# Kernel tuning notes

Measured on AMD Instinct MI355X. Metric: run time of the kernel, lower is better.

## Reference

```python
import jax, jax.numpy as jnp
import numpy as np

N, E, IN, HID, OUT, H, R = 50000, 800000, 128, 64, 64, 4, 64
NEG_SLOPE = 0.2


def setup_inputs() -> dict:
    key = jax.random.key(0)
    ks = jax.random.split(key, 20)
    s = 0.05
    inp = {
        "x": jax.random.normal(ks[0], (N, IN), jnp.float32),
        "edge_index": jax.random.randint(ks[1], (2, E), 0, N, jnp.int32),
        "edge_type": jax.random.randint(ks[2], (E,), 0, R, jnp.int32),
        # layer 1 (in -> hidden)
        "rel1": jax.random.normal(ks[3], (R, IN), jnp.float32) * s,
        "W1": jax.random.normal(ks[4], (IN, H * HID), jnp.float32) * s,
        "We1": jax.random.normal(ks[5], (IN, H * HID), jnp.float32) * s,
        "as1": jax.random.normal(ks[6], (H, HID), jnp.float32) * s,
        "ad1": jax.random.normal(ks[7], (H, HID), jnp.float32) * s,
        "ae1": jax.random.normal(ks[8], (H, HID), jnp.float32) * s,
        "b1": jnp.zeros((HID,), jnp.float32),
        # layer 2 (hidden -> out)
        "rel2": jax.random.normal(ks[9], (R, HID), jnp.float32) * s,
        "W2": jax.random.normal(ks[10], (HID, H * OUT), jnp.float32) * s,
        "We2": jax.random.normal(ks[11], (HID, H * OUT), jnp.float32) * s,
        "as2": jax.random.normal(ks[12], (H, OUT), jnp.float32) * s,
        "ad2": jax.random.normal(ks[13], (H, OUT), jnp.float32) * s,
        "ae2": jax.random.normal(ks[14], (H, OUT), jnp.float32) * s,
        "b2": jnp.zeros((OUT,), jnp.float32),
    }
    return inp


def gat_layer(x, src, dst, edge_type, rel, W, We, a_s, a_d, a_e, b, C):
    # x: [N, Din] -> per-head features [N, H, C]
    xs = (x @ W).reshape(-1, H, C)
    alpha_src = jnp.einsum('nhc,hc->nh', xs, a_s)   # [N,H]
    alpha_dst = jnp.einsum('nhc,hc->nh', xs, a_d)   # [N,H]
    e = (rel[edge_type] @ We).reshape(-1, H, C)     # [E,H,C] projected edge feats
    alpha_e = jnp.einsum('ehc,hc->eh', e, a_e)      # [E,H]
    logits = alpha_src[src] + alpha_dst[dst] + alpha_e
    logits = jnp.where(logits >= 0, logits, NEG_SLOPE * logits)  # leaky_relu
    # segment softmax over destination nodes
    lmax = jax.ops.segment_max(logits, dst, num_segments=N)      # [N,H]
    ex = jnp.exp(logits - lmax[dst])
    den = jax.ops.segment_sum(ex, dst, num_segments=N)           # [N,H]
    w = ex / den[dst]                                            # [E,H]
    msg = w[:, :, None] * xs[src]                                # [E,H,C]
    out = jax.ops.segment_sum(msg, dst, num_segments=N)          # [N,H,C]
    return out.mean(axis=1) + b                                  # concat=False -> head mean


def reference(x, edge_index, edge_type, rel1, W1, We1, as1, ad1, ae1, b1,
              rel2, W2, We2, as2, ad2, ae2, b2):
    src, dst = edge_index[0], edge_index[1]
    h = gat_layer(x, src, dst, edge_type, rel1, W1, We1, as1, ad1, ae1, b1, HID)
    h = jax.nn.relu(h)
    out = gat_layer(h, src, dst, edge_type, rel2, W2, We2, as2, ad2, ae2, b2, OUT)
    return out
```

## Files before the change

### kernel.cpp

```cpp
#include <hip/hip_runtime.h>
#include <hip/hip_bf16.h>
#include <hip/hip_fp16.h>
#include <math.h>

#define N_NODES 50000
#define N_EDGES 800000
#define IN_DIM 128
#define NHEAD 4
#define NREL 64
#define HC 256
#define NEG_SLOPE 0.2f
#define SCAN_B ((N_NODES + 255) / 256)
#define XB (N_NODES / 16)
#define HB ((N_EDGES + 255) / 256)

using short8 = __attribute__((ext_vector_type(8))) short;
using f32x4  = __attribute__((ext_vector_type(4))) float;

__device__ __forceinline__ void load_lds16s(const short* g, short* l) {
  __builtin_amdgcn_global_load_lds(
      (const __attribute__((address_space(1))) unsigned int*)g,
      (__attribute__((address_space(3))) unsigned int*)l, 16, 0, 0);
}

__device__ __forceinline__ unsigned bf16rne(float v) {
  unsigned u = __float_as_uint(v);
  return (u + 0x7FFFu + ((u >> 16) & 1u)) >> 16;
}

__global__ __launch_bounds__(256) void fused_prep(
    const float* __restrict__ x, short* __restrict__ xfh, short* __restrict__ xfl,
    const int* __restrict__ dst, int* __restrict__ deg,
    const float* __restrict__ rel1, const float* __restrict__ We1, const float* __restrict__ ae1,
    const float* __restrict__ rel2, const float* __restrict__ We2, const float* __restrict__ ae2,
    float* __restrict__ tab1, float* __restrict__ tab2,
    const float* __restrict__ W1, short* __restrict__ w1h, short* __restrict__ w1l,
    const float* __restrict__ W2, short* __restrict__ w2h, short* __restrict__ w2l) {
  const int bid = blockIdx.x;
  const int t = threadIdx.x;
  __shared__ float plds[16 * 132];

  if (bid < XB) {
    const int K = IN_DIM, LW = K + 4;
    for (int i = t * 4; i < 16 * K; i += 1024) {
      int r = i / K, k = i - r * K;
      *(float4*)&plds[r * LW + k] = *(const float4*)&x[(size_t)(bid * 16 + r) * K + k];
    }
    __syncthreads();
    for (int c = t; c < 2 * K; c += 256) {
      int p_k = c >> 6, l = c & 63;
      int r = l & 15, k0 = p_k * 32 + (l >> 4) * 8;
      unsigned hp[4], lp[4];
#pragma unroll
      for (int q = 0; q < 4; ++q) {
        float v0 = plds[r * LW + k0 + q * 2];
        float v1 = plds[r * LW + k0 + q * 2 + 1];
        unsigned h0 = bf16rne(v0), h1 = bf16rne(v1);
        float l0 = (v0 - __uint_as_float(h0 << 16)) * 256.0f;
        float l1 = (v1 - __uint_as_float(h1 << 16)) * 256.0f;
        hp[q] = h0 | (h1 << 16);
        lp[q] = bf16rne(l0) | (bf16rne(l1) << 16);
      }
      size_t base = ((size_t)(bid * (K >> 5) + p_k) * 64 + l) * 8;
      *(int4*)&xfh[base] = make_int4(hp[0], hp[1], hp[2], hp[3]);
      *(int4*)&xfl[base] = make_int4(lp[0], lp[1], lp[2], lp[3]);
    }
    return;
  }
  if (bid < XB + HB) {
    const int e = (bid - XB) * 256 + t;
    if (e < N_EDGES) atomicAdd(&deg[dst[e]], 1);
    return;
  }
  if (bid < XB + HB + 128) {
    const int rb = bid - (XB + HB);
    const int layer = rb >> 6, r = rb & 63;
    const float* rel = layer ? rel2 : rel1;
    const float* We  = layer ? We2  : We1;
    const float* ae  = layer ? ae2  : ae1;
    float* tab       = layer ? tab2 : tab1;
    const int K      = layer ? 64   : IN_DIM;
    float acc = 0.f;
    for (int k = 0; k < K; ++k) acc += rel[(size_t)r * K + k] * We[(size_t)k * HC + t];
    int h = t >> 6, lane = t & 63;
    float p = acc * ae[t];
#pragma unroll
    for (int off = 32; off > 0; off >>= 1) p += __shfl_down(p, off);
    if (lane == 0) tab[r * NHEAD + h] = p;
    return;
  }
  {
    const int wb = bid - (XB + HB + 128);
    const float* W; short* Wh; short* Wl; int K, c;
    if (wb < 16) { W = W1; Wh = w1h; Wl = w1l; K = IN_DIM; c = wb * 256 + t; }
    else         { W = W2; Wh = w2h; Wl = w2l; K = 64;     c = (wb - 16) * 256 + t; }
    const int KP = K >> 5;
    if (c >= 16 * KP * 64) return;
    const int p = c >> 6, l = c & 63;
    const int p_c = p / KP, p_k = p - p_c * KP;
    const int col = p_c * 16 + (l & 15), k0 = p_k * 32 + (l >> 4) * 8;
    unsigned hp[4], lp[4];
#pragma unroll
    for (int q = 0; q < 4; ++q) {
      float v0 = W[(size_t)(k0 + q * 2) * HC + col];
      float v1 = W[(size_t)(k0 + q * 2 + 1) * HC + col];
      unsigned h0 = bf16rne(v0), h1 = bf16rne(v1);
      float l0 = (v0 - __uint_as_float(h0 << 16)) * 256.0f;
      float l1 = (v1 - __uint_as_float(h1 << 16)) * 256.0f;
      hp[q] = h0 | (h1 << 16);
      lp[q] = bf16rne(l0) | (bf16rne(l1) << 16);
    }
    size_t base = (size_t)c * 8;
    *(int4*)&Wh[base] = make_int4(hp[0], hp[1], hp[2], hp[3]);
    *(int4*)&Wl[base] = make_int4(lp[0], lp[1], lp[2], lp[3]);
  }
}

__global__ __launch_bounds__(256, 4) void gemm_mfma(
    const short* __restrict__ Xh, const short* __restrict__ Xl,
    const short* __restrict__ Wh, const short* __restrict__ Wl,
    const float* __restrict__ a_s, const float* __restrict__ a_d,
    __half2* __restrict__ xs16, float* __restrict__ asrc, float* __restrict__ adst,
    int M, int K) {
  __shared__ short lds[2][24 * 512];
  const int t = threadIdx.x;
  const int wv = t >> 6, l = t & 63;
  const int KP = K >> 5;
  const int pr0 = blockIdx.x * 4;
  const int pc0 = blockIdx.y * 8;
  const int c0 = blockIdx.y * 128;

#define STAGE(BI, PK)                                                         \
  {                                                                           \
    _Pragma("unroll")                                                         \
    for (int j = 0; j < 6; ++j) {                                             \
      const int s = wv * 6 + j;                                               \
      const short* srcp;                                                      \
      if (s < 4)       srcp = Xh + (((size_t)(pr0 + s) * KP + (PK)) << 9);    \
      else if (s < 8)  srcp = Xl + (((size_t)(pr0 + s - 4) * KP + (PK)) << 9);\
      else if (s < 16) srcp = Wh + (((size_t)(pc0 + s - 8) * KP + (PK)) << 9);\
      else             srcp = Wl + (((size_t)(pc0 + s - 16) * KP + (PK)) << 9);\
      load_lds16s(srcp + l * 8, &lds[BI][s * 512]);                           \
    }                                                                         \
  }

  f32x4 acc0[8], acc1[8];
#pragma unroll
  for (int i = 0; i < 8; ++i)
#pragma unroll
    for (int c = 0; c < 4; ++c) { acc0[i][c] = 0.f; acc1[i][c] = 0.f; }

  STAGE(0, 0);
  for (int pk = 0; pk < KP; ++pk) {
    const int cur = pk & 1;
    if (pk + 1 < KP) {
      STAGE(cur ^ 1, pk + 1);
      asm volatile("s_waitcnt vmcnt(6)" ::: "memory");
    } else {
      asm volatile("s_waitcnt vmcnt(0)" ::: "memory");
    }
    __builtin_amdgcn_s_barrier();
    __builtin_amdgcn_sched_barrier(0);
    const short8 ah = *(const short8*)&lds[cur][(0 + wv) * 512 + l * 8];
    const short8 al = *(const short8*)&lds[cur][(4 + wv) * 512 + l * 8];
#pragma unroll
    for (int t8 = 0; t8 < 8; ++t8) {
      const short8 bh = *(const short8*)&lds[cur][(8 + t8) * 512 + l * 8];
      const short8 bl = *(const short8*)&lds[cur][(16 + t8) * 512 + l * 8];
      acc0[t8] = __builtin_amdgcn_mfma_f32_16x16x32_bf16(ah, bh, acc0[t8], 0, 0, 0);
      acc1[t8] = __builtin_amdgcn_mfma_f32_16x16x32_bf16(ah, bl, acc1[t8], 0, 0, 0);
      acc1[t8] = __builtin_amdgcn_mfma_f32_16x16x32_bf16(al, bh, acc1[t8], 0, 0, 0);
    }
    asm volatile("" ::: "memory");
    __builtin_amdgcn_s_barrier();
  }
#undef STAGE

  const int col_l = l & 15;
  const int row_l = (l >> 4) * 4;
  __half* xsh = (__half*)xs16;
  float asv[8], adv[8];
#pragma unroll
  for (int t8 = 0; t8 < 8; ++t8) {
    asv[t8] = a_s[c0 + t8 * 16 + col_l];
    adv[t8] = a_d[c0 + t8 * 16 + col_l];
  }
  float sp[2][4], dp[2][4];
#pragma unroll
  for (int hl = 0; hl < 2; ++hl)
#pragma unroll
    for (int r = 0; r < 4; ++r) { sp[hl][r] = 0.f; dp[hl][r] = 0.f; }

#pragma unroll
  for (int t8 = 0; t8 < 8; ++t8) {
    const int hl = t8 >> 2;
#pragma unroll
    for (int r = 0; r < 4; ++r) {
      const float v = acc0[t8][r] + acc1[t8][r] * (1.0f / 256.0f);
      const int row = (pr0 + wv) * 16 + row_l + r;
      if (row < M) {
        const int col = c0 + t8 * 16 + col_l;
        xsh[(size_t)row * HC + col] = __float2half(v);
      }
      sp[hl][r] += v * asv[t8];
      dp[hl][r] += v * adv[t8];
    }
  }
#pragma unroll
  for (int off = 1; off < 16; off <<= 1) {
#pragma unroll
    for (int hl = 0; hl < 2; ++hl)
#pragma unroll
      for (int r = 0; r < 4; ++r) {
        sp[hl][r] += __shfl_xor(sp[hl][r], off);
        dp[hl][r] += __shfl_xor(dp[hl][r], off);
      }
  }
  if (col_l == 0) {
#pragma unroll
    for (int hl = 0; hl < 2; ++hl) {
      const int head = blockIdx.y * 2 + hl;
#pragma unroll
      for (int r = 0; r < 4; ++r) {
        const int row = (pr0 + wv) * 16 + row_l + r;
        if (row < M) {
          asrc[row * NHEAD + head] = sp[hl][r];
          adst[row * NHEAD + head] = dp[hl][r];
        }
      }
    }
  }
}

__global__ __launch_bounds__(256) void block_sum_kernel(
    const int* __restrict__ deg, int* __restrict__ bsum) {
  int i = blockIdx.x * 256 + threadIdx.x;
  int v = (i < N_NODES) ? deg[i] : 0;
#pragma unroll
  for (int off = 32; off > 0; off >>= 1) v += __shfl_down(v, off);
  __shared__ int w[4];
  if ((threadIdx.x & 63) == 0) w[threadIdx.x >> 6] = v;
  __syncthreads();
  if (threadIdx.x == 0) bsum[blockIdx.x] = w[0] + w[1] + w[2] + w[3];
}

__global__ __launch_bounds__(256) void scan_bsum_kernel(
    const int* __restrict__ bsum, int* __restrict__ boff) {
  __shared__ int s[256];
  int t = threadIdx.x;
  int v = (t < SCAN_B) ? bsum[t] : 0;
  s[t] = v;
  __syncthreads();
  for (int off = 1; off < 256; off <<= 1) {
    int u = (t >= off) ? s[t - off] : 0;
    __syncthreads();
    s[t] += u;
    __syncthreads();
  }
  boff[t] = (t == 0) ? 0 : s[t - 1];
}

__global__ __launch_bounds__(256) void scan_final_kernel(
    const int* __restrict__ deg, const int* __restrict__ boff,
    int* __restrict__ rowptr, int* __restrict__ cursor) {
  __shared__ int s[256];
  int t = threadIdx.x;
  int i = blockIdx.x * 256 + t;
  int v = (i < N_NODES) ? deg[i] : 0;
  s[t] = v;
  __syncthreads();
  for (int off = 1; off < 256; off <<= 1) {
    int u = (t >= off) ? s[t - off] : 0;
    __syncthreads();
    s[t] += u;
    __syncthreads();
  }
  int excl = boff[blockIdx.x] + s[t] - v;
  if (i < N_NODES) {
    rowptr[i] = excl;
    cursor[i] = excl;
  }
  if (t == 0 && blockIdx.x == 0) rowptr[N_NODES] = N_EDGES;
}

__global__ __launch_bounds__(256) void fill_kernel(
    const int* __restrict__ src, const int* __restrict__ dst,
    const int* __restrict__ etype, int* __restrict__ cursor,
    int2* __restrict__ csr_pack) {
  int e = blockIdx.x * blockDim.x + threadIdx.x;
  if (e >= N_EDGES) return;
  int d = dst[e];
  int i = atomicAdd(&cursor[d], 1);
  csr_pack[i] = make_int2(src[e], etype[e]);
}

__global__ __launch_bounds__(256) void gat_node_kernel(
    const int* __restrict__ rowptr, const int2* __restrict__ csr,
    const float* __restrict__ asrc, const float* __restrict__ adst,
    const float* __restrict__ tab, const __half2* __restrict__ xs16,
    const float* __restrict__ b, float* __restrict__ out,
    short* __restrict__ oxh, short* __restrict__ oxl, int mode) {
  const int n = (blockIdx.x * blockDim.x + threadIdx.x) >> 6;
  if (n >= N_NODES) return;
  const int lane = threadIdx.x & 63;
  const int hh = lane >> 4;
  const int cbase = lane << 2;
  const int i0 = rowptr[n], i1 = rowptr[n + 1];
  const float adn = adst[n * NHEAD + hh];
  const float treg = tab[lane * NHEAD + hh];

  float4 acc = make_float4(0.f, 0.f, 0.f, 0.f);
  float den = 0.f;
  int i = i0;
  for (; i + 4 <= i1; i += 4) {
    const int2 p0 = csr[i], p1 = csr[i + 1], p2 = csr[i + 2], p3 = csr[i + 3];
    float l0 = asrc[p0.x * NHEAD + hh] + adn + __shfl(treg, p0.y);
    float l1 = asrc[p1.x * NHEAD + hh] + adn + __shfl(treg, p1.y);
    float l2 = asrc[p2.x * NHEAD + hh] + adn + __shfl(treg, p2.y);
    float l3 = asrc[p3.x * NHEAD + hh] + adn + __shfl(treg, p3.y);
    const uint2 q0 = *(const uint2*)&xs16[((size_t)p0.x * HC + cbase) >> 1];
    const uint2 q1 = *(const uint2*)&xs16[((size_t)p1.x * HC + cbase) >> 1];
    const uint2 q2 = *(const uint2*)&xs16[((size_t)p2.x * HC + cbase) >> 1];
    const uint2 q3 = *(const uint2*)&xs16[((size_t)p3.x * HC + cbase) >> 1];
    l0 = (l0 >= 0.f) ? l0 : NEG_SLOPE * l0;
    l1 = (l1 >= 0.f) ? l1 : NEG_SLOPE * l1;
    l2 = (l2 >= 0.f) ? l2 : NEG_SLOPE * l2;
    l3 = (l3 >= 0.f) ? l3 : NEG_SLOPE * l3;
    const float w0 = __expf(l0), w1 = __expf(l1), w2 = __expf(l2), w3 = __expf(l3);
    den += (w0 + w1) + (w2 + w3);
    const float2 a0 = __half22float2(*(const __half2*)&q0.x), b0 = __half22float2(*(const __half2*)&q0.y);
    const float2 a1 = __half22float2(*(const __half2*)&q1.x), b1 = __half22float2(*(const __half2*)&q1.y);
    const float2 a2 = __half22float2(*(const __half2*)&q2.x), b2 = __half22float2(*(const __half2*)&q2.y);
    const float2 a3 = __half22float2(*(const __half2*)&q3.x), b3 = __half22float2(*(const __half2*)&q3.y);
    acc.x += w0 * a0.x + w1 * a1.x + w2 * a2.x + w3 * a3.x;
    acc.y += w0 * a0.y + w1 * a1.y + w2 * a2.y + w3 * a3.y;
    acc.z += w0 * b0.x + w1 * b1.x + w2 * b2.x + w3 * b3.x;
    acc.w += w0 * b0.y + w1 * b1.y + w2 * b2.y + w3 * b3.y;
  }
  for (; i < i1; ++i) {
    const int2 p = csr[i];
    float l = asrc[p.x * NHEAD + hh] + adn + __shfl(treg, p.y);
    l = (l >= 0.f) ? l : NEG_SLOPE * l;
    const float w = __expf(l);
    const uint2 q = *(const uint2*)&xs16[((size_t)p.x * HC + cbase) >> 1];
    const float2 a = __half22float2(*(const __half2*)&q.x);
    const float2 c = __half22float2(*(const __half2*)&q.y);
    den += w;
    acc.x += w * a.x; acc.y += w * a.y; acc.z += w * c.x; acc.w += w * c.y;
  }

  const float rd = (den > 0.f) ? (0.25f / den) : 0.f;
  float4 y = make_float4(acc.x * rd, acc.y * rd, acc.z * rd, acc.w * rd);
#pragma unroll
  for (int off = 16; off < 64; off <<= 1) {
    y.x += __shfl_xor(y.x, off);
    y.y += __shfl_xor(y.y, off);
    y.z += __shfl_xor(y.z, off);
    y.w += __shfl_xor(y.w, off);
  }
  if (lane < 16) {
    const float4 bb = *(const float4*)&b[lane * 4];
    y.x += bb.x; y.y += bb.y; y.z += bb.z; y.w += bb.w;
    if (mode) {
      y.x = fmaxf(y.x, 0.f); y.y = fmaxf(y.y, 0.f);
      y.z = fmaxf(y.z, 0.f); y.w = fmaxf(y.w, 0.f);
      unsigned h0 = bf16rne(y.x), h1 = bf16rne(y.y);
      unsigned h2 = bf16rne(y.z), h3 = bf16rne(y.w);
      float l0 = (y.x - __uint_as_float(h0 << 16)) * 256.0f;
      float l1 = (y.y - __uint_as_float(h1 << 16)) * 256.0f;
      float l2 = (y.z - __uint_as_float(h2 << 16)) * 256.0f;
      float l3 = (y.w - __uint_as_float(h3 << 16)) * 256.0f;
      unsigned hp0 = h0 | (h1 << 16), hp1 = h2 | (h3 << 16);
      unsigned lp0 = bf16rne(l0) | (bf16rne(l1) << 16);
      unsigned lp1 = bf16rne(l2) | (bf16rne(l3) << 16);
      const int pk = lane >> 3;
      const int lip = (n & 15) + ((lane >> 1) & 3) * 16;
      const int j0 = (lane & 1) * 4;
      size_t base = ((size_t)((n >> 4) * 2 + pk) * 64 + lip) * 8 + j0;
      *(uint2*)&oxh[base] = make_uint2(hp0, hp1);
      *(uint2*)&oxl[base] = make_uint2(lp0, lp1);
    } else {
      *(float4*)&out[(size_t)n * 64 + lane * 4] = y;
    }
  }
}

extern "C" void kernel_launch(void* const* d_in, const int* in_sizes, int n_in,
                              void* d_out, int out_size, void* d_ws, size_t ws_size,
                              hipStream_t stream) {
  const float* x   = (const float*)d_in[0];
  const int* eidx  = (const int*)d_in[1];
  const int* etype = (const int*)d_in[2];
  const float* rel1 = (const float*)d_in[3];
  const float* W1   = (const float*)d_in[4];
  const float* We1  = (const float*)d_in[5];
  const float* as1  = (const float*)d_in[6];
  const float* ad1  = (const float*)d_in[7];
  const float* ae1  = (const float*)d_in[8];
  const float* b1   = (const float*)d_in[9];
  const float* rel2 = (const float*)d_in[10];
  const float* W2   = (const float*)d_in[11];
  const float* We2  = (const float*)d_in[12];
  const float* as2  = (const float*)d_in[13];
  const float* ad2  = (const float*)d_in[14];
  const float* ae2  = (const float*)d_in[15];
  const float* b2   = (const float*)d_in[16];
  const int* src = eidx;
  const int* dst = eidx + N_EDGES;

  char* wsb = (char*)d_ws;
  size_t off = 0;
  auto carve = [&](size_t bytes) { char* p = wsb + off; off = (off + bytes + 255) & ~(size_t)255; return p; };
  __half2* xs16 = (__half2*)carve((size_t)N_NODES * HC * 2);
  float* asrc = (float*)carve((size_t)N_NODES * NHEAD * 4);
  float* adst = (float*)carve((size_t)N_NODES * NHEAD * 4);
  float* tab1 = (float*)carve(NREL * NHEAD * 4);
  float* tab2 = (float*)carve(NREL * NHEAD * 4);
  short* xfh  = (short*)carve(((size_t)N_NODES * IN_DIM + 32768) * 2);
  short* xfl  = (short*)carve(((size_t)N_NODES * IN_DIM + 32768) * 2);
  short* w1h  = (short*)carve(256 * IN_DIM * 2);
  short* w1l  = (short*)carve(256 * IN_DIM * 2);
  short* w2h  = (short*)carve(256 * 64 * 2);
  short* w2l  = (short*)carve(256 * 64 * 2);
  int* deg    = (int*)carve(N_NODES * 4);
  int* rowptr = (int*)carve((N_NODES + 1) * 4);
  int* cursor = (int*)carve(N_NODES * 4);
  int2* csr   = (int2*)carve((size_t)N_EDGES * 8);
  int* bsum   = (int*)carve(256 * 4);
  int* boff   = (int*)carve(256 * 4);

  hipMemsetAsync(deg, 0, N_NODES * sizeof(int), stream);

  fused_prep<<<XB + HB + 128 + 16 + 8, 256, 0, stream>>>(
      x, xfh, xfl, dst, deg,
      rel1, We1, ae1, rel2, We2, ae2, tab1, tab2,
      W1, w1h, w1l, W2, w2h, w2l);

  block_sum_kernel<<<SCAN_B, 256, 0, stream>>>(deg, bsum);
  scan_bsum_kernel<<<1, 256, 0, stream>>>(bsum, boff);
  scan_final_kernel<<<SCAN_B, 256, 0, stream>>>(deg, boff, rowptr, cursor);
  fill_kernel<<<HB, 256, 0, stream>>>(src, dst, etype, cursor, csr);

  const dim3 gemm_grid((N_NODES + 63) / 64, 2);
  const int GB = (N_NODES * 64 + 255) / 256;

  gemm_mfma<<<gemm_grid, 256, 0, stream>>>(xfh, xfl, w1h, w1l, as1, ad1, xs16, asrc, adst, N_NODES, IN_DIM);
  gat_node_kernel<<<GB, 256, 0, stream>>>(rowptr, csr, asrc, adst, tab1, xs16,
                                          b1, nullptr, xfh, xfl, 1);

  gemm_mfma<<<gemm_grid, 256, 0, stream>>>(xfh, xfl, w2h, w2l, as2, ad2, xs16, asrc, adst, N_NODES, 64);
  gat_node_kernel<<<GB, 256, 0, stream>>>(rowptr, csr, asrc, adst, tab2, xs16,
                                          b2, (float*)d_out, nullptr, nullptr, 0);
}
```

Baseline: 302.8 us.

## Record per-edge rank in histogram pass and pack CSR entries into 32 bits

```diff
diff --git a/kernel.cpp b/kernel.cpp
--- a/kernel.cpp
+++ b/kernel.cpp
@@ -28,9 +28,18 @@
   return (u + 0x7FFFu + ((u >> 16) & 1u)) >> 16;
 }
 
+__global__ __launch_bounds__(256) void hist_rank_kernel(
+    const int* __restrict__ dst, int* __restrict__ deg,
+    unsigned short* __restrict__ rank) {
+  int e = blockIdx.x * blockDim.x + threadIdx.x;
+  if (e < N_EDGES) {
+    int r = atomicAdd(&deg[dst[e]], 1);
+    rank[e] = (unsigned short)r;
+  }
+}
+
 __global__ __launch_bounds__(256) void fused_prep(
     const float* __restrict__ x, short* __restrict__ xfh, short* __restrict__ xfl,
-    const int* __restrict__ dst, int* __restrict__ deg,
     const float* __restrict__ rel1, const float* __restrict__ We1, const float* __restrict__ ae1,
     const float* __restrict__ rel2, const float* __restrict__ We2, const float* __restrict__ ae2,
     float* __restrict__ tab1, float* __restrict__ tab2,
@@ -67,13 +76,8 @@
     }
     return;
   }
-  if (bid < XB + HB) {
-    const int e = (bid - XB) * 256 + t;
-    if (e < N_EDGES) atomicAdd(&deg[dst[e]], 1);
-    return;
-  }
-  if (bid < XB + HB + 128) {
-    const int rb = bid - (XB + HB);
+  if (bid < XB + 128) {
+    const int rb = bid - XB;
     const int layer = rb >> 6, r = rb & 63;
     const float* rel = layer ? rel2 : rel1;
     const float* We  = layer ? We2  : We1;
@@ -90,7 +94,7 @@
     return;
   }
   {
-    const int wb = bid - (XB + HB + 128);
+    const int wb = bid - (XB + 128);
     const float* W; short* Wh; short* Wl; int K, c;
     if (wb < 16) { W = W1; Wh = w1h; Wl = w1l; K = IN_DIM; c = wb * 256 + t; }
     else         { W = W2; Wh = w2h; Wl = w2l; K = 64;     c = (wb - 16) * 256 + t; }
@@ -262,7 +266,7 @@
 
 __global__ __launch_bounds__(256) void scan_final_kernel(
     const int* __restrict__ deg, const int* __restrict__ boff,
-    int* __restrict__ rowptr, int* __restrict__ cursor) {
+    int* __restrict__ rowptr) {
   __shared__ int s[256];
   int t = threadIdx.x;
   int i = blockIdx.x * 256 + t;
@@ -276,26 +280,23 @@
     __syncthreads();
   }
   int excl = boff[blockIdx.x] + s[t] - v;
-  if (i < N_NODES) {
-    rowptr[i] = excl;
-    cursor[i] = excl;
-  }
+  if (i < N_NODES) rowptr[i] = excl;
   if (t == 0 && blockIdx.x == 0) rowptr[N_NODES] = N_EDGES;
 }
 
 __global__ __launch_bounds__(256) void fill_kernel(
     const int* __restrict__ src, const int* __restrict__ dst,
-    const int* __restrict__ etype, int* __restrict__ cursor,
-    int2* __restrict__ csr_pack) {
+    const int* __restrict__ etype, const unsigned short* __restrict__ rank,
+    const int* __restrict__ rowptr, int* __restrict__ csrp) {
   int e = blockIdx.x * blockDim.x + threadIdx.x;
   if (e >= N_EDGES) return;
   int d = dst[e];
-  int i = atomicAdd(&cursor[d], 1);
-  csr_pack[i] = make_int2(src[e], etype[e]);
+  int pos = rowptr[d] + rank[e];
+  csrp[pos] = src[e] | (etype[e] << 16);
 }
 
 __global__ __launch_bounds__(256) void gat_node_kernel(
-    const int* __restrict__ rowptr, const int2* __restrict__ csr,
+    const int* __restrict__ rowptr, const int* __restrict__ csr,
     const float* __restrict__ asrc, const float* __restrict__ adst,
     const float* __restrict__ tab, const __half2* __restrict__ xs16,
     const float* __restrict__ b, float* __restrict__ out,
@@ -313,15 +314,16 @@
   float den = 0.f;
   int i = i0;
   for (; i + 4 <= i1; i += 4) {
-    const int2 p0 = csr[i], p1 = csr[i + 1], p2 = csr[i + 2], p3 = csr[i + 3];
-    float l0 = asrc[p0.x * NHEAD + hh] + adn + __shfl(treg, p0.y);
-    float l1 = asrc[p1.x * NHEAD + hh] + adn + __shfl(treg, p1.y);
-    float l2 = asrc[p2.x * NHEAD + hh] + adn + __shfl(treg, p2.y);
-    float l3 = asrc[p3.x * NHEAD + hh] + adn + __shfl(treg, p3.y);
-    const uint2 q0 = *(const uint2*)&xs16[((size_t)p0.x * HC + cbase) >> 1];
-    const uint2 q1 = *(const uint2*)&xs16[((size_t)p1.x * HC + cbase) >> 1];
-    const uint2 q2 = *(const uint2*)&xs16[((size_t)p2.x * HC + cbase) >> 1];
-    const uint2 q3 = *(const uint2*)&xs16[((size_t)p3.x * HC + cbase) >> 1];
+    const int p0 = csr[i], p1 = csr[i + 1], p2 = csr[i + 2], p3 = csr[i + 3];
+    const int s0 = p0 & 0xFFFF, s1 = p1 & 0xFFFF, s2 = p2 & 0xFFFF, s3 = p3 & 0xFFFF;
+    float l0 = asrc[s0 * NHEAD + hh] + adn + __shfl(treg, p0 >> 16);
+    float l1 = asrc[s1 * NHEAD + hh] + adn + __shfl(treg, p1 >> 16);
+    float l2 = asrc[s2 * NHEAD + hh] + adn + __shfl(treg, p2 >> 16);
+    float l3 = asrc[s3 * NHEAD + hh] + adn + __shfl(treg, p3 >> 16);
+    const uint2 q0 = *(const uint2*)&xs16[((size_t)s0 * HC + cbase) >> 1];
+    const uint2 q1 = *(const uint2*)&xs16[((size_t)s1 * HC + cbase) >> 1];
+    const uint2 q2 = *(const uint2*)&xs16[((size_t)s2 * HC + cbase) >> 1];
+    const uint2 q3 = *(const uint2*)&xs16[((size_t)s3 * HC + cbase) >> 1];
     l0 = (l0 >= 0.f) ? l0 : NEG_SLOPE * l0;
     l1 = (l1 >= 0.f) ? l1 : NEG_SLOPE * l1;
     l2 = (l2 >= 0.f) ? l2 : NEG_SLOPE * l2;
@@ -338,11 +340,12 @@
     acc.w += w0 * b0.y + w1 * b1.y + w2 * b2.y + w3 * b3.y;
   }
   for (; i < i1; ++i) {
-    const int2 p = csr[i];
-    float l = asrc[p.x * NHEAD + hh] + adn + __shfl(treg, p.y);
+    const int p = csr[i];
+    const int s = p & 0xFFFF;
+    float l = asrc[s * NHEAD + hh] + adn + __shfl(treg, p >> 16);
     l = (l >= 0.f) ? l : NEG_SLOPE * l;
     const float w = __expf(l);
-    const uint2 q = *(const uint2*)&xs16[((size_t)p.x * HC + cbase) >> 1];
+    const uint2 q = *(const uint2*)&xs16[((size_t)s * HC + cbase) >> 1];
     const float2 a = __half22float2(*(const __half2*)&q.x);
     const float2 c = __half22float2(*(const __half2*)&q.y);
     den += w;
@@ -424,31 +427,33 @@
   short* w2l  = (short*)carve(256 * 64 * 2);
   int* deg    = (int*)carve(N_NODES * 4);
   int* rowptr = (int*)carve((N_NODES + 1) * 4);
-  int* cursor = (int*)carve(N_NODES * 4);
-  int2* csr   = (int2*)carve((size_t)N_EDGES * 8);
+  unsigned short* rank = (unsigned short*)carve((size_t)N_EDGES * 2);
+  int* csrp   = (int*)carve((size_t)N_EDGES * 4);
   int* bsum   = (int*)carve(256 * 4);
   int* boff   = (int*)carve(256 * 4);
 
   hipMemsetAsync(deg, 0, N_NODES * sizeof(int), stream);
 
-  fused_prep<<<XB + HB + 128 + 16 + 8, 256, 0, stream>>>(
-      x, xfh, xfl, dst, deg,
+  hist_rank_kernel<<<HB, 256, 0, stream>>>(dst, deg, rank);
+
+  fused_prep<<<XB + 128 + 16 + 8, 256, 0, stream>>>(
+      x, xfh, xfl,
       rel1, We1, ae1, rel2, We2, ae2, tab1, tab2,
       W1, w1h, w1l, W2, w2h, w2l);
 
   block_sum_kernel<<<SCAN_B, 256, 0, stream>>>(deg, bsum);
   scan_bsum_kernel<<<1, 256, 0, stream>>>(bsum, boff);
-  scan_final_kernel<<<SCAN_B, 256, 0, stream>>>(deg, boff, rowptr, cursor);
-  fill_kernel<<<HB, 256, 0, stream>>>(src, dst, etype, cursor, csr);
+  scan_final_kernel<<<SCAN_B, 256, 0, stream>>>(deg, boff, rowptr);
+  fill_kernel<<<HB, 256, 0, stream>>>(src, dst, etype, rank, rowptr, csrp);
 
   const dim3 gemm_grid((N_NODES + 63) / 64, 2);
   const int GB = (N_NODES * 64 + 255) / 256;
 
   gemm_mfma<<<gemm_grid, 256, 0, stream>>>(xfh, xfl, w1h, w1l, as1, ad1, xs16, asrc, adst, N_NODES, IN_DIM);
-  gat_node_kernel<<<GB, 256, 0, stream>>>(rowptr, csr, asrc, adst, tab1, xs16,
+  gat_node_kernel<<<GB, 256, 0, stream>>>(rowptr, csrp, asrc, adst, tab1, xs16,
                                           b1, nullptr, xfh, xfl, 1);
 
   gemm_mfma<<<gemm_grid, 256, 0, stream>>>(xfh, xfl, w2h, w2l, as2, ad2, xs16, asrc, adst, N_NODES, 64);
-  gat_node_kernel<<<GB, 256, 0, stream>>>(rowptr, csr, asrc, adst, tab2, xs16,
+  gat_node_kernel<<<GB, 256, 0, stream>>>(rowptr, csrp, asrc, adst, tab2, xs16,
                                           b2, (float*)d_out, nullptr, nullptr, 0);
 }
```

Result: faster. 273.2 us (median of 2 runs) (-9.8%).
